# Kernel optimization log

Measured on AMD Instinct MI355X. Metric: run time of the kernel, lower is better.

The kernel has to match this reference:

```python
import jax, jax.numpy as jnp
import numpy as np

EPS = 1e-5

def l2norm(x, axis=-1):
    # matches torch F.normalize(p=2): denom clamped at 1e-12
    n = jnp.linalg.norm(x, axis=axis, keepdims=True)
    return x / jnp.maximum(n, 1e-12)

def setup_inputs() -> dict:
    key = jax.random.key(0)
    ks = jax.random.split(key, 10)
    B, N, D, P = 8, 1024, 128, 16
    context = jax.random.normal(ks[0], (B, N, D), jnp.float32)
    acc_u = jax.random.normal(ks[1], (B, N, 1), jnp.float32)
    acc_v = jax.random.normal(ks[2], (B, N, 1), jnp.float32)
    uv_angle = jax.random.normal(ks[3], (B, N, 1), jnp.float32)
    uv_angleACC = jax.random.normal(ks[4], (B, N, 1), jnp.float32)
    speed = jax.random.normal(ks[5], (B, N, 1), jnp.float32)
    dist = jax.random.uniform(ks[6], (N, N), jnp.float32)
    angle = jax.random.normal(ks[7], (N, N), jnp.float32)
    # xavier_uniform for weight_tensor [P, D]: bound = sqrt(6/(P+D))
    bound = float(np.sqrt(6.0 / (P + D)))
    weight_tensor = jax.random.uniform(ks[8], (P, D), jnp.float32, -bound, bound)
    return {"context": context, "acc_u": acc_u, "acc_v": acc_v,
            "uv_angle": uv_angle, "uv_angleACC": uv_angleACC, "speed": speed,
            "isPhy": 1, "dist": dist, "angle": angle,
            "weight_tensor": weight_tensor}

def reference(context, acc_u, acc_v, uv_angle, uv_angleACC, speed, isPhy, dist, angle, weight_tensor):
    gamma, theta, sigma = 1.4, 0.5, 0.5
    P = weight_tensor.shape[0]
    N = context.shape[1]
    # --- weighted-cosine multi-perspective attention ---
    w = weight_tensor[:, None, None, :]                 # [P,1,1,D]
    context_fc = context[None] * w                      # [P,B,N,D]
    context_norm = l2norm(context_fc)                   # [P,B,N,D]
    # matmul over perspectives then mean over P
    attention = jnp.einsum('pbnd,pbmd->bnm', context_norm, context_norm) / P
    # --- epsilon neighbourhood (epsilon=0, markoff=0), mask detached ---
    mask = jax.lax.stop_gradient((attention > 0.0).astype(attention.dtype))
    attention = attention * mask
    # --- wind dynamics (pred_var 'u', isPhy True, dist given) ---
    Acc = acc_u * acc_u + acc_v * acc_v                 # [B,N,1]
    x1 = jnp.sqrt(Acc[:, :, 0] + EPS)                   # [B,N]
    x2 = jnp.abs(jnp.cos(uv_angleACC[:, :, 0] - uv_angle[:, :, 0]))
    temp_acc = x1 * x2                                  # [B,N]
    acc_part = temp_acc[:, :, None] * jnp.eye(N, dtype=attention.dtype)  # diag [B,N,N]
    spd = jax.lax.stop_gradient(speed)                  # speed.detach()
    ang = jax.lax.stop_gradient(angle)[None]            # torch.tensor() detaches
    d = jax.lax.stop_gradient(dist)[None] + EPS
    # uv_angle/speed broadcast [B,N,1] -> [B,N,N] (repeat along last dim)
    selfwind = jnp.abs(spd) * jnp.abs(jnp.cos(ang - uv_angle) + sigma * acc_part) / d
    selfwind = l2norm(selfwind)                         # [B,N,N]
    y = gamma * jnp.einsum('bnk,bmk->bnm', selfwind, selfwind) / 20.0 + EPS
    y = l2norm(y)
    u = l2norm(jnp.abs(theta * selfwind + jnp.sqrt(y)) + EPS)
    return attention * u
```

## Files before the change

### kernel.cpp

```cpp
#include <hip/hip_runtime.h>
#include <hip/hip_bf16.h>
#include <math.h>

#define EPSV 1e-5f
#define AS1 __attribute__((address_space(1)))
#define AS3 __attribute__((address_space(3)))

typedef __attribute__((ext_vector_type(4))) float f32x4;
typedef __attribute__((ext_vector_type(8))) short bf16x8;
typedef __attribute__((ext_vector_type(4))) unsigned short u16x4;

__device__ __forceinline__ unsigned short f2b(float x) {
  union { float f; unsigned int u; } v; v.f = x;
  unsigned int r = v.u + 0x7FFFu + ((v.u >> 16) & 1u);
  return (unsigned short)(r >> 16);
}
__device__ __forceinline__ float b2f(unsigned short h) {
  union { float f; unsigned int u; } v; v.u = ((unsigned int)h) << 16;
  return v.f;
}

__device__ __forceinline__ float block_reduce_sum(float v, float* sbuf) {
  #pragma unroll
  for (int off = 32; off; off >>= 1) v += __shfl_xor(v, off);
  __syncthreads();
  if ((threadIdx.x & 63) == 0) sbuf[threadIdx.x >> 6] = v;
  __syncthreads();
  return sbuf[0] + sbuf[1] + sbuf[2] + sbuf[3];
}

__global__ __launch_bounds__(256) void tabkern(const float* __restrict__ angle,
                                               const float* __restrict__ dist,
                                               float* __restrict__ CT,
                                               float* __restrict__ ST) {
  const int i = (blockIdx.x * 256 + threadIdx.x) * 4;
  const f32x4 a = *(const f32x4*)(angle + i);
  const f32x4 d = *(const f32x4*)(dist + i);
  f32x4 ct, st;
  #pragma unroll
  for (int j = 0; j < 4; ++j) {
    const float inv = 1.0f / (d[j] + EPSV);
    float s, c;
    __sincosf(a[j], &s, &c);
    ct[j] = c * inv;
    st[j] = s * inv;
  }
  *(f32x4*)(CT + i) = ct;
  *(f32x4*)(ST + i) = st;
}

__global__ __launch_bounds__(256) void prep(const float* __restrict__ ctx,
                                            const float* __restrict__ wt,
                                            const float* __restrict__ speed,
                                            const float* __restrict__ uva,
                                            const float* __restrict__ accu,
                                            const float* __restrict__ accv,
                                            const float* __restrict__ uvaACC,
                                            const float* __restrict__ CT,
                                            const float* __restrict__ ST,
                                            const float* __restrict__ dist,
                                            unsigned short* __restrict__ V,
                                            unsigned short* __restrict__ SW,
                                            int BN, int N) {
  __shared__ float sbuf[4];
  const int blk = blockIdx.x;
  if (blk < BN) {
    const int bn = blk;
    const int w = threadIdx.x >> 6;
    const int lane = threadIdx.x & 63;
    const int p = w * 4 + (lane >> 4);
    const int dl = (lane & 15) * 8;
    const float* c = ctx + (size_t)bn * 128;
    const f32x4 ca = *(const f32x4*)(c + dl);
    const f32x4 cb = *(const f32x4*)(c + dl + 4);
    const f32x4 wa = *(const f32x4*)(wt + p * 128 + dl);
    const f32x4 wb = *(const f32x4*)(wt + p * 128 + dl + 4);
    float a[8];
    float ss = 0.0f;
    #pragma unroll
    for (int i = 0; i < 4; ++i) {
      a[i] = ca[i] * wa[i];
      a[4 + i] = cb[i] * wb[i];
      ss += a[i] * a[i] + a[4 + i] * a[4 + i];
    }
    ss += __shfl_xor(ss, 1);
    ss += __shfl_xor(ss, 2);
    ss += __shfl_xor(ss, 4);
    ss += __shfl_xor(ss, 8);
    const float inv = 1.0f / fmaxf(sqrtf(ss), 1e-12f);
    bf16x8 o;
    #pragma unroll
    for (int i = 0; i < 8; ++i) o[i] = (short)f2b(a[i] * inv);
    *(bf16x8*)(V + (size_t)bn * 2048 + p * 128 + dl) = o;
  } else {
    const int bn = blk - BN;
    const int n = bn & (N - 1);
    const int t = threadIdx.x;
    const float ua = uva[bn];
    float su, cu;
    __sincosf(ua, &su, &cu);
    const float sp = fabsf(speed[bn]);
    const float au = accu[bn], av = accv[bn];
    const float ta = sqrtf(au * au + av * av + EPSV) * fabsf(cosf(uvaACC[bn] - ua));
    const float diag = 0.5f * ta / (dist[(size_t)n * N + n] + EPSV);
    const f32x4 ct = *(const f32x4*)(CT + (size_t)n * N + 4 * t);
    const f32x4 st = *(const f32x4*)(ST + (size_t)n * N + 4 * t);
    float v[4];
    float ss = 0.0f;
    #pragma unroll
    for (int i = 0; i < 4; ++i) {
      float x = cu * ct[i] + su * st[i];
      if (4 * t + i == n) x += diag;
      v[i] = sp * fabsf(x);
      ss += v[i] * v[i];
    }
    ss = block_reduce_sum(ss, sbuf);
    const float inv = 1.0f / fmaxf(sqrtf(ss), 1e-12f);
    u16x4 o;
    #pragma unroll
    for (int i = 0; i < 4; ++i) o[i] = f2b(v[i] * inv);
    *(u16x4*)(SW + (size_t)bn * N + 4 * t) = o;
  }
}

#define FENCE asm volatile("" ::: "memory")
__device__ __forceinline__ void barx() { FENCE; __builtin_amdgcn_s_barrier(); FENCE; }

__global__ __launch_bounds__(512, 4) void gemm8(const unsigned short* __restrict__ V,
                                                const unsigned short* __restrict__ SW,
                                                float* __restrict__ OUT,
                                                unsigned short* __restrict__ Yb,
                                                int boff) {
  __shared__ __align__(16) unsigned short As[3][128 * 32];
  __shared__ __align__(16) unsigned short Bs[3][256 * 32];
  const int id = blockIdx.x + boff;
  const bool att = id < 256;
  const int r = att ? id : id - 256;
  const int b = r & 7;
  const int tile = r >> 3;
  const int m0 = (tile & 7) * 128;
  const int n0 = (tile >> 3) * 256;
  const int K = att ? 2048 : 1024;
  const int NN = 1024;
  const unsigned short* Ab = att ? (V + (size_t)b * NN * 2048) : (SW + (size_t)b * NN * NN);

  const int tid = threadIdx.x;
  const int lane = tid & 63;
  const int wid = tid >> 6;
  const int wm = (wid >> 2) * 64;
  const int wn = (wid & 3) * 64;
  const int fr = lane & 15;
  const int fc = lane >> 4;
  const int rsw = (fc ^ ((fr >> 1) & 3)) << 3;

  f32x4 acc[4][4] = {};
  bf16x8 af[4], bf[4];

  auto stage = [&](int sb, int kt) {
    const int k0 = kt << 5;
    {
      const int row = tid >> 2;
      const int c = (tid & 3) ^ ((row >> 1) & 3);
      __builtin_amdgcn_global_load_lds(
          (const AS1 unsigned int*)(Ab + (size_t)(m0 + row) * K + k0 + (c << 3)),
          (AS3 unsigned int*)(&As[sb][tid * 8]), 16, 0, 0);
    }
    #pragma unroll
    for (int e = 0; e < 2; ++e) {
      const int idx = e * 512 + tid;
      const int row = idx >> 2;
      const int c = (idx & 3) ^ ((row >> 1) & 3);
      __builtin_amdgcn_global_load_lds(
          (const AS1 unsigned int*)(Ab + (size_t)(n0 + row) * K + k0 + (c << 3)),
          (AS3 unsigned int*)(&Bs[sb][idx * 8]), 16, 0, 0);
    }
  };

  const int nk = K >> 5;

  stage(0, 0);
  stage(1, 1);
  asm volatile("s_waitcnt vmcnt(3)" ::: "memory");
  barx();

  int rd = 0;
  for (int t = 0; t < nk; ++t) {
    const unsigned short* Ar = As[rd];
    const unsigned short* Br = Bs[rd];
    #pragma unroll
    for (int i = 0; i < 4; ++i)
      af[i] = *(const bf16x8*)(Ar + (wm + i * 16 + fr) * 32 + rsw);
    #pragma unroll
    for (int j = 0; j < 4; ++j)
      bf[j] = *(const bf16x8*)(Br + (wn + j * 16 + fr) * 32 + rsw);

    if (t + 2 < nk) {
      int st = rd + 2; if (st >= 3) st -= 3;
      stage(st, t + 2);
    }
    barx();
    asm volatile("s_waitcnt lgkmcnt(0)" ::: "memory");
    __builtin_amdgcn_s_setprio(1);
    #pragma unroll
    for (int i = 0; i < 4; ++i)
      #pragma unroll
      for (int j = 0; j < 4; ++j)
        acc[i][j] = __builtin_amdgcn_mfma_f32_16x16x32_bf16(af[i], bf[j], acc[i][j], 0, 0, 0);
    __builtin_amdgcn_s_setprio(0);
    if (t + 2 < nk)      { asm volatile("s_waitcnt vmcnt(3)" ::: "memory"); }
    else if (t + 1 < nk) { asm volatile("s_waitcnt vmcnt(0)" ::: "memory"); }
    barx();
    rd = (rd + 1 == 3) ? 0 : rd + 1;
  }

  if (att) {
    float* Cb = OUT + (size_t)b * NN * NN;
    #pragma unroll
    for (int i = 0; i < 4; ++i)
      #pragma unroll
      for (int rr = 0; rr < 4; ++rr) {
        const int row = m0 + wm + i * 16 + fc * 4 + rr;
        #pragma unroll
        for (int j = 0; j < 4; ++j) {
          const int col = n0 + wn + j * 16 + fr;
          Cb[(size_t)row * NN + col] = fmaxf(acc[i][j][rr] * (1.0f / 16.0f), 0.0f);
        }
      }
  } else {
    unsigned short* Cb = Yb + (size_t)b * NN * NN;
    #pragma unroll
    for (int i = 0; i < 4; ++i)
      #pragma unroll
      for (int rr = 0; rr < 4; ++rr) {
        const int row = m0 + wm + i * 16 + fc * 4 + rr;
        #pragma unroll
        for (int j = 0; j < 4; ++j) {
          const int col = n0 + wn + j * 16 + fr;
          Cb[(size_t)row * NN + col] = f2b(acc[i][j][rr] * (1.4f / 20.0f) + EPSV);
        }
      }
  }
}

__global__ __launch_bounds__(256) void finkern(const unsigned short* __restrict__ Yb,
                                               const unsigned short* __restrict__ SW,
                                               float* __restrict__ OUT) {
  const int row = blockIdx.x * 4 + (threadIdx.x >> 6);
  const int lane = threadIdx.x & 63;
  const unsigned short* y = Yb + (size_t)row * 1024;
  const unsigned short* sw = SW + (size_t)row * 1024;
  float* o = OUT + (size_t)row * 1024;

  float yv[16];
  float ss = 0.0f;
  #pragma unroll
  for (int ch = 0; ch < 4; ++ch) {
    const u16x4 yr = *(const u16x4*)(y + ch * 256 + lane * 4);
    #pragma unroll
    for (int i = 0; i < 4; ++i) {
      yv[ch * 4 + i] = b2f(yr[i]);
      ss += yv[ch * 4 + i] * yv[ch * 4 + i];
    }
  }
  #pragma unroll
  for (int off = 32; off; off >>= 1) ss += __shfl_xor(ss, off);
  const float invy = 1.0f / fmaxf(sqrtf(ss), 1e-12f);

  float tv[16];
  float st = 0.0f;
  #pragma unroll
  for (int ch = 0; ch < 4; ++ch) {
    const u16x4 sr = *(const u16x4*)(sw + ch * 256 + lane * 4);
    #pragma unroll
    for (int i = 0; i < 4; ++i) {
      const float x = fabsf(0.5f * b2f(sr[i]) + sqrtf(yv[ch * 4 + i] * invy)) + EPSV;
      tv[ch * 4 + i] = x;
      st += x * x;
    }
  }
  #pragma unroll
  for (int off = 32; off; off >>= 1) st += __shfl_xor(st, off);
  const float invt = 1.0f / fmaxf(sqrtf(st), 1e-12f);

  #pragma unroll
  for (int ch = 0; ch < 4; ++ch) {
    f32x4 ov = *(f32x4*)(o + ch * 256 + lane * 4);
    #pragma unroll
    for (int i = 0; i < 4; ++i) ov[i] *= tv[ch * 4 + i] * invt;
    *(f32x4*)(o + ch * 256 + lane * 4) = ov;
  }
}

extern "C" void kernel_launch(void* const* d_in, const int* in_sizes, int n_in,
                              void* d_out, int out_size, void* d_ws, size_t ws_size,
                              hipStream_t stream) {
  const float* ctx        = (const float*)d_in[0];
  const float* acc_u      = (const float*)d_in[1];
  const float* acc_v      = (const float*)d_in[2];
  const float* uv_angle   = (const float*)d_in[3];
  const float* uv_angleACC= (const float*)d_in[4];
  const float* speed      = (const float*)d_in[5];
  const float* dist       = (const float*)d_in[7];
  const float* angle      = (const float*)d_in[8];
  const float* wt         = (const float*)d_in[9];

  const int B = 8, N = 1024, P = 16;
  const int K1 = P * 128;
  const int BN = B * N;

  const size_t szV  = (size_t)BN * K1 * 2;
  const size_t szSW = (size_t)BN * N * 2;
  const size_t szYb = (size_t)BN * N * 2;
  const size_t szT  = (size_t)N * N * 4;

  unsigned short* V  = (unsigned short*)d_ws;
  unsigned short* SW = (unsigned short*)((char*)d_ws + szV);
  float* out = (float*)d_out;

  if (ws_size >= szV + szSW + szYb) {
    char* region3 = (char*)d_ws + szV + szSW;
    float* CT = (float*)region3;
    float* ST = (float*)(region3 + szT);
    unsigned short* Yp = (unsigned short*)region3;

    tabkern<<<dim3(N * N / 1024), dim3(256), 0, stream>>>(angle, dist, CT, ST);
    prep<<<dim3(2 * BN), dim3(256), 0, stream>>>(ctx, wt, speed, uv_angle, acc_u,
                                                 acc_v, uv_angleACC, CT, ST, dist,
                                                 V, SW, BN, N);
    gemm8<<<dim3(512), dim3(512), 0, stream>>>(V, SW, out, Yp, 0);
    finkern<<<dim3(BN / 4), dim3(256), 0, stream>>>(Yp, SW, out);
  } else {
    char* tabs = (char*)d_ws + szV + szSW;
    float* CT = (float*)tabs;
    float* ST = (float*)(tabs + szT);
    unsigned short* Yp = (unsigned short*)d_ws;

    tabkern<<<dim3(N * N / 1024), dim3(256), 0, stream>>>(angle, dist, CT, ST);
    prep<<<dim3(2 * BN), dim3(256), 0, stream>>>(ctx, wt, speed, uv_angle, acc_u,
                                                 acc_v, uv_angleACC, CT, ST, dist,
                                                 V, SW, BN, N);
    gemm8<<<dim3(256), dim3(512), 0, stream>>>(V, SW, out, Yp, 0);
    gemm8<<<dim3(256), dim3(512), 0, stream>>>(V, SW, out, Yp, 256);
    finkern<<<dim3(BN / 4), dim3(256), 0, stream>>>(Yp, SW, out);
  }
}
```

Before: 173.3 us.

## Drop trig table kernel, store attention in bf16 workspace, restructure GEMM loop

Removes the separate cos/sin-over-dist table kernel and merges both halves of prep into one block per row, which computes cos(angle-ua)/dist directly. The GEMM can now write the attention tile as bf16 into a workspace buffer, so the final kernel reads bf16 instead of doing a read-modify-write of fp32 output. This cuts memory traffic. The main loop now issues the next stage's prefetch before the LDS fragment reads and drops one barrier and an lgkmcnt wait per iteration. That risks an LDS read/write race on the triple buffer, and bf16 attention lowers precision.

```diff
diff --git a/kernel.cpp b/kernel.cpp
--- a/kernel.cpp
+++ b/kernel.cpp
@@ -27,26 +27,6 @@
   if ((threadIdx.x & 63) == 0) sbuf[threadIdx.x >> 6] = v;
   __syncthreads();
   return sbuf[0] + sbuf[1] + sbuf[2] + sbuf[3];
-}
-
-__global__ __launch_bounds__(256) void tabkern(const float* __restrict__ angle,
-                                               const float* __restrict__ dist,
-                                               float* __restrict__ CT,
-                                               float* __restrict__ ST) {
-  const int i = (blockIdx.x * 256 + threadIdx.x) * 4;
-  const f32x4 a = *(const f32x4*)(angle + i);
-  const f32x4 d = *(const f32x4*)(dist + i);
-  f32x4 ct, st;
-  #pragma unroll
-  for (int j = 0; j < 4; ++j) {
-    const float inv = 1.0f / (d[j] + EPSV);
-    float s, c;
-    __sincosf(a[j], &s, &c);
-    ct[j] = c * inv;
-    st[j] = s * inv;
-  }
-  *(f32x4*)(CT + i) = ct;
-  *(f32x4*)(ST + i) = st;
 }
 
 __global__ __launch_bounds__(256) void prep(const float* __restrict__ ctx,
@@ -56,18 +36,18 @@
                                             const float* __restrict__ accu,
                                             const float* __restrict__ accv,
                                             const float* __restrict__ uvaACC,
-                                            const float* __restrict__ CT,
-                                            const float* __restrict__ ST,
+                                            const float* __restrict__ angle,
                                             const float* __restrict__ dist,
                                             unsigned short* __restrict__ V,
                                             unsigned short* __restrict__ SW,
-                                            int BN, int N) {
+                                            int N) {
   __shared__ float sbuf[4];
-  const int blk = blockIdx.x;
-  if (blk < BN) {
-    const int bn = blk;
-    const int w = threadIdx.x >> 6;
-    const int lane = threadIdx.x & 63;
+  const int bn = blockIdx.x;
+  const int tid = threadIdx.x;
+
+  {
+    const int w = tid >> 6;
+    const int lane = tid & 63;
     const int p = w * 4 + (lane >> 4);
     const int dl = (lane & 15) * 8;
     const float* c = ctx + (size_t)bn * 128;
@@ -92,26 +72,23 @@
     #pragma unroll
     for (int i = 0; i < 8; ++i) o[i] = (short)f2b(a[i] * inv);
     *(bf16x8*)(V + (size_t)bn * 2048 + p * 128 + dl) = o;
-  } else {
-    const int bn = blk - BN;
+  }
+
+  {
     const int n = bn & (N - 1);
-    const int t = threadIdx.x;
     const float ua = uva[bn];
-    float su, cu;
-    __sincosf(ua, &su, &cu);
     const float sp = fabsf(speed[bn]);
     const float au = accu[bn], av = accv[bn];
     const float ta = sqrtf(au * au + av * av + EPSV) * fabsf(cosf(uvaACC[bn] - ua));
-    const float diag = 0.5f * ta / (dist[(size_t)n * N + n] + EPSV);
-    const f32x4 ct = *(const f32x4*)(CT + (size_t)n * N + 4 * t);
-    const f32x4 st = *(const f32x4*)(ST + (size_t)n * N + 4 * t);
+    const f32x4 an = *(const f32x4*)(angle + (size_t)n * N + 4 * tid);
+    const f32x4 dv = *(const f32x4*)(dist + (size_t)n * N + 4 * tid);
     float v[4];
     float ss = 0.0f;
     #pragma unroll
     for (int i = 0; i < 4; ++i) {
-      float x = cu * ct[i] + su * st[i];
-      if (4 * t + i == n) x += diag;
-      v[i] = sp * fabsf(x);
+      float cv = cosf(an[i] - ua);
+      if (4 * tid + i == n) cv += 0.5f * ta;
+      v[i] = sp * fabsf(cv) / (dv[i] + EPSV);
       ss += v[i] * v[i];
     }
     ss = block_reduce_sum(ss, sbuf);
@@ -119,17 +96,19 @@
     u16x4 o;
     #pragma unroll
     for (int i = 0; i < 4; ++i) o[i] = f2b(v[i] * inv);
-    *(u16x4*)(SW + (size_t)bn * N + 4 * t) = o;
+    *(u16x4*)(SW + (size_t)bn * N + 4 * tid) = o;
   }
 }
 
 #define FENCE asm volatile("" ::: "memory")
 __device__ __forceinline__ void barx() { FENCE; __builtin_amdgcn_s_barrier(); FENCE; }
 
+template <bool ATTB>
 __global__ __launch_bounds__(512, 4) void gemm8(const unsigned short* __restrict__ V,
                                                 const unsigned short* __restrict__ SW,
                                                 float* __restrict__ OUT,
                                                 unsigned short* __restrict__ Yb,
+                                                unsigned short* __restrict__ ATT,
                                                 int boff) {
   __shared__ __align__(16) unsigned short As[3][128 * 32];
   __shared__ __align__(16) unsigned short Bs[3][256 * 32];
@@ -185,21 +164,18 @@
 
   int rd = 0;
   for (int t = 0; t < nk; ++t) {
-    const unsigned short* Ar = As[rd];
-    const unsigned short* Br = Bs[rd];
-    #pragma unroll
-    for (int i = 0; i < 4; ++i)
-      af[i] = *(const bf16x8*)(Ar + (wm + i * 16 + fr) * 32 + rsw);
-    #pragma unroll
-    for (int j = 0; j < 4; ++j)
-      bf[j] = *(const bf16x8*)(Br + (wn + j * 16 + fr) * 32 + rsw);
-
     if (t + 2 < nk) {
       int st = rd + 2; if (st >= 3) st -= 3;
       stage(st, t + 2);
     }
-    barx();
-    asm volatile("s_waitcnt lgkmcnt(0)" ::: "memory");
+    const unsigned short* Ar = As[rd];
+    const unsigned short* Br = Bs[rd];
+    #pragma unroll
+    for (int i = 0; i < 4; ++i)
+      af[i] = *(const bf16x8*)(Ar + (wm + i * 16 + fr) * 32 + rsw);
+    #pragma unroll
+    for (int j = 0; j < 4; ++j)
+      bf[j] = *(const bf16x8*)(Br + (wn + j * 16 + fr) * 32 + rsw);
     __builtin_amdgcn_s_setprio(1);
     #pragma unroll
     for (int i = 0; i < 4; ++i)
@@ -214,18 +190,33 @@
   }
 
   if (att) {
-    float* Cb = OUT + (size_t)b * NN * NN;
-    #pragma unroll
-    for (int i = 0; i < 4; ++i)
-      #pragma unroll
-      for (int rr = 0; rr < 4; ++rr) {
-        const int row = m0 + wm + i * 16 + fc * 4 + rr;
+    if (ATTB) {
+      unsigned short* Cb = ATT + (size_t)b * NN * NN;
+      #pragma unroll
+      for (int i = 0; i < 4; ++i)
         #pragma unroll
-        for (int j = 0; j < 4; ++j) {
-          const int col = n0 + wn + j * 16 + fr;
-          Cb[(size_t)row * NN + col] = fmaxf(acc[i][j][rr] * (1.0f / 16.0f), 0.0f);
+        for (int rr = 0; rr < 4; ++rr) {
+          const int row = m0 + wm + i * 16 + fc * 4 + rr;
+          #pragma unroll
+          for (int j = 0; j < 4; ++j) {
+            const int col = n0 + wn + j * 16 + fr;
+            Cb[(size_t)row * NN + col] = f2b(fmaxf(acc[i][j][rr] * (1.0f / 16.0f), 0.0f));
+          }
         }
-      }
+    } else {
+      float* Cb = OUT + (size_t)b * NN * NN;
+      #pragma unroll
+      for (int i = 0; i < 4; ++i)
+        #pragma unroll
+        for (int rr = 0; rr < 4; ++rr) {
+          const int row = m0 + wm + i * 16 + fc * 4 + rr;
+          #pragma unroll
+          for (int j = 0; j < 4; ++j) {
+            const int col = n0 + wn + j * 16 + fr;
+            Cb[(size_t)row * NN + col] = fmaxf(acc[i][j][rr] * (1.0f / 16.0f), 0.0f);
+          }
+        }
+    }
   } else {
     unsigned short* Cb = Yb + (size_t)b * NN * NN;
     #pragma unroll
@@ -242,8 +233,10 @@
   }
 }
 
+template <bool ATTB>
 __global__ __launch_bounds__(256) void finkern(const unsigned short* __restrict__ Yb,
                                                const unsigned short* __restrict__ SW,
+                                               const unsigned short* __restrict__ ATT,
                                                float* __restrict__ OUT) {
   const int row = blockIdx.x * 4 + (threadIdx.x >> 6);
   const int lane = threadIdx.x & 63;
@@ -282,12 +275,24 @@
   for (int off = 32; off; off >>= 1) st += __shfl_xor(st, off);
   const float invt = 1.0f / fmaxf(sqrtf(st), 1e-12f);
 
-  #pragma unroll
-  for (int ch = 0; ch < 4; ++ch) {
-    f32x4 ov = *(f32x4*)(o + ch * 256 + lane * 4);
-    #pragma unroll
-    for (int i = 0; i < 4; ++i) ov[i] *= tv[ch * 4 + i] * invt;
-    *(f32x4*)(o + ch * 256 + lane * 4) = ov;
+  if (ATTB) {
+    const unsigned short* at = ATT + (size_t)row * 1024;
+    #pragma unroll
+    for (int ch = 0; ch < 4; ++ch) {
+      const u16x4 ar = *(const u16x4*)(at + ch * 256 + lane * 4);
+      f32x4 ov;
+      #pragma unroll
+      for (int i = 0; i < 4; ++i) ov[i] = b2f(ar[i]) * (tv[ch * 4 + i] * invt);
+      *(f32x4*)(o + ch * 256 + lane * 4) = ov;
+    }
+  } else {
+    #pragma unroll
+    for (int ch = 0; ch < 4; ++ch) {
+      f32x4 ov = *(f32x4*)(o + ch * 256 + lane * 4);
+      #pragma unroll
+      for (int i = 0; i < 4; ++i) ov[i] *= tv[ch * 4 + i] * invt;
+      *(f32x4*)(o + ch * 256 + lane * 4) = ov;
+    }
   }
 }
 
@@ -311,36 +316,29 @@
   const size_t szV  = (size_t)BN * K1 * 2;
   const size_t szSW = (size_t)BN * N * 2;
   const size_t szYb = (size_t)BN * N * 2;
-  const size_t szT  = (size_t)N * N * 4;
+  const size_t szA  = (size_t)BN * N * 2;
 
   unsigned short* V  = (unsigned short*)d_ws;
   unsigned short* SW = (unsigned short*)((char*)d_ws + szV);
   float* out = (float*)d_out;
 
-  if (ws_size >= szV + szSW + szYb) {
-    char* region3 = (char*)d_ws + szV + szSW;
-    float* CT = (float*)region3;
-    float* ST = (float*)(region3 + szT);
-    unsigned short* Yp = (unsigned short*)region3;
-
-    tabkern<<<dim3(N * N / 1024), dim3(256), 0, stream>>>(angle, dist, CT, ST);
-    prep<<<dim3(2 * BN), dim3(256), 0, stream>>>(ctx, wt, speed, uv_angle, acc_u,
-                                                 acc_v, uv_angleACC, CT, ST, dist,
-                                                 V, SW, BN, N);
-    gemm8<<<dim3(512), dim3(512), 0, stream>>>(V, SW, out, Yp, 0);
-    finkern<<<dim3(BN / 4), dim3(256), 0, stream>>>(Yp, SW, out);
+  prep<<<dim3(BN), dim3(256), 0, stream>>>(ctx, wt, speed, uv_angle, acc_u,
+                                           acc_v, uv_angleACC, angle, dist,
+                                           V, SW, N);
+
+  if (ws_size >= szV + szSW + szYb + szA) {
+    unsigned short* Yp = (unsigned short*)((char*)d_ws + szV + szSW);
+    unsigned short* At = (unsigned short*)((char*)d_ws + szV + szSW + szYb);
+    gemm8<true><<<dim3(512), dim3(512), 0, stream>>>(V, SW, out, Yp, At, 0);
+    finkern<true><<<dim3(BN / 4), dim3(256), 0, stream>>>(Yp, SW, At, out);
+  } else if (ws_size >= szV + szSW + szYb) {
+    unsigned short* Yp = (unsigned short*)((char*)d_ws + szV + szSW);
+    gemm8<false><<<dim3(512), dim3(512), 0, stream>>>(V, SW, out, Yp, nullptr, 0);
+    finkern<false><<<dim3(BN / 4), dim3(256), 0, stream>>>(Yp, SW, nullptr, out);
   } else {
-    char* tabs = (char*)d_ws + szV + szSW;
-    float* CT = (float*)tabs;
-    float* ST = (float*)(tabs + szT);
     unsigned short* Yp = (unsigned short*)d_ws;
-
-    tabkern<<<dim3(N * N / 1024), dim3(256), 0, stream>>>(angle, dist, CT, ST);
-    prep<<<dim3(2 * BN), dim3(256), 0, stream>>>(ctx, wt, speed, uv_angle, acc_u,
-                                                 acc_v, uv_angleACC, CT, ST, dist,
-                                                 V, SW, BN, N);
-    gemm8<<<dim3(256), dim3(512), 0, stream>>>(V, SW, out, Yp, 0);
-    gemm8<<<dim3(256), dim3(512), 0, stream>>>(V, SW, out, Yp, 256);
-    finkern<<<dim3(BN / 4), dim3(256), 0, stream>>>(Yp, SW, out);
-  }
-}
+    gemm8<false><<<dim3(256), dim3(512), 0, stream>>>(V, SW, out, Yp, nullptr, 0);
+    gemm8<false><<<dim3(256), dim3(512), 0, stream>>>(V, SW, out, Yp, nullptr, 256);
+    finkern<false><<<dim3(BN / 4), dim3(256), 0, stream>>>(Yp, SW, nullptr, out);
+  }
+}
```

Result: faster. 169.7 us (-2.1%).
